# Kernel optimization log

Hardware: AMD Instinct MI355X
Metric: run time of the kernel (lower is better)

## Reference

```python
import jax, jax.numpy as jnp
import numpy as np

# Real spherical harmonics constants (torch-ngp / instant-ngp shencoder convention)
C0 = 0.28209479177387814
C1 = 0.48860251190291987
C2_0 = 1.0925484305920792
C2_2 = 0.94617469575755997
C2_2b = 0.31539156525251999
C2_4 = 0.54627421529603959
C3_0 = 0.59004358992664352
C3_1 = 2.8906114426405538
C3_2 = 0.45704579946446572
C3_3 = 0.3731763325901154
C3_5 = 1.4453057213202769


def sh_encode_deg4(d):
    # d: [..., 3] normalized directions -> [..., 16]
    x, y, z = d[..., 0], d[..., 1], d[..., 2]
    x2, y2, z2 = x * x, y * y, z * z
    xy, yz, xz = x * y, y * z, x * z
    terms = [
        jnp.full_like(x, C0),            # l=0
        -C1 * y,                          # l=1
        C1 * z,
        -C1 * x,
        C2_0 * xy,                        # l=2
        -C2_0 * yz,
        C2_2 * z2 - C2_2b,
        -C2_0 * xz,
        C2_4 * (x2 - y2),
        C3_0 * y * (-3.0 * x2 + y2),      # l=3
        C3_1 * xy * z,
        C3_2 * y * (1.0 - 5.0 * z2),
        C3_3 * z * (5.0 * z2 - 3.0),
        C3_2 * x * (1.0 - 5.0 * z2),
        C3_5 * z * (x2 - y2),
        C3_0 * x * (-x2 + 3.0 * y2),
    ]
    return jnp.stack(terms, axis=-1)


def setup_inputs() -> dict:
    key = jax.random.key(0)
    d = jax.random.normal(key, (4194304, 3), dtype=jnp.float32)
    d = d / jnp.linalg.norm(d, axis=-1, keepdims=True)  # module expects normalized dirs
    return {"direction": d}


def reference(direction):
    # SHEncoder.forward with degree=4: [..., 3] -> [..., 16]
    prefix = direction.shape[:-1]
    out = sh_encode_deg4(direction.reshape(-1, 3))
    return out.reshape(prefix + (16,))
```

## Files before the change

kernel.cpp:

```cpp
#include <hip/hip_runtime.h>
#include <hip/hip_bf16.h>


#define C0    0.28209479177387814f
#define C1    0.48860251190291987f
#define C2_0  1.0925484305920792f
#define C2_2  0.94617469575755997f
#define C2_2b 0.31539156525251999f
#define C2_4  0.54627421529603959f
#define C3_0  0.59004358992664352f
#define C3_1  2.8906114426405538f
#define C3_2  0.45704579946446572f
#define C3_3  0.3731763325901154f
#define C3_5  1.4453057213202769f

#define BLK 256

__global__ __launch_bounds__(BLK) void sh_encode_kernel(
    const float* __restrict__ din, float* __restrict__ dout, int N) {
    __shared__ float4 s4[BLK * 4];

    const int tid  = threadIdx.x;
    const int base = blockIdx.x * BLK;
    const int i    = base + tid;

    float x = 0.f, y = 0.f, z = 0.f;
    if (i < N) {
        const float* p = din + (size_t)3 * i;
        x = p[0]; y = p[1]; z = p[2];
    }

    const float x2 = x * x, y2 = y * y, z2 = z * z;
    const float xy = x * y, yz = y * z, xz = x * z;

    float t[16];
    t[0]  = C0;
    t[1]  = -C1 * y;
    t[2]  =  C1 * z;
    t[3]  = -C1 * x;
    t[4]  =  C2_0 * xy;
    t[5]  = -C2_0 * yz;
    t[6]  =  C2_2 * z2 - C2_2b;
    t[7]  = -C2_0 * xz;
    t[8]  =  C2_4 * (x2 - y2);
    t[9]  =  C3_0 * y * (-3.0f * x2 + y2);
    t[10] =  C3_1 * xy * z;
    t[11] =  C3_2 * y * (1.0f - 5.0f * z2);
    t[12] =  C3_3 * z * (5.0f * z2 - 3.0f);
    t[13] =  C3_2 * x * (1.0f - 5.0f * z2);
    t[14] =  C3_5 * z * (x2 - y2);
    t[15] =  C3_0 * x * (-x2 + 3.0f * y2);

    const int sw = (tid >> 1) & 3;
    #pragma unroll
    for (int g = 0; g < 4; ++g) {
        s4[tid * 4 + (g ^ sw)] =
            make_float4(t[4 * g], t[4 * g + 1], t[4 * g + 2], t[4 * g + 3]);
    }

    __syncthreads();

    float4* outb4 = (float4*)(dout + (size_t)base * 16);
    #pragma unroll
    for (int it = 0; it < 4; ++it) {
        const int e4 = it * BLK + tid;
        const int p  = e4 >> 2;
        const int q  = e4 & 3;
        if (base + p < N)
            outb4[e4] = s4[p * 4 + (q ^ ((p >> 1) & 3))];
    }
}

extern "C" void kernel_launch(void* const* d_in, const int* in_sizes, int n_in,
                              void* d_out, int out_size, void* d_ws, size_t ws_size,
                              hipStream_t stream) {
    const float* din = (const float*)d_in[0];
    float* dout      = (float*)d_out;
    const int N      = in_sizes[0] / 3;
    const int blocks = (N + BLK - 1) / BLK;
    sh_encode_kernel<<<blocks, BLK, 0, stream>>>(din, dout, N);
}
```

Measured before the change: 57.84 us.

## Use per-wave LDS transpose, nontemporal stores, and drop block barrier

Each wave now stages and transposes only its own 64 points in a private slice of shared memory, so the block-wide __syncthreads is replaced by a wave-local LDS wait. Output stores use nontemporal hints so the large streaming write bypasses cache retention, and full blocks skip the per-element bounds checks. The approach relies on wave-level lockstep for LDS visibility, which holds for 64-wide AMD waves but is an implicit assumption.

```diff
diff --git a/kernel.cpp b/kernel.cpp
--- a/kernel.cpp
+++ b/kernel.cpp
@@ -16,16 +16,21 @@
 
 #define BLK 256
 
+typedef float f4 __attribute__((ext_vector_type(4)));
+
 __global__ __launch_bounds__(BLK) void sh_encode_kernel(
     const float* __restrict__ din, float* __restrict__ dout, int N) {
-    __shared__ float4 s4[BLK * 4];
+    __shared__ f4 s4[BLK * 4];
 
     const int tid  = threadIdx.x;
+    const int lane = tid & 63;
+    const int wave = tid >> 6;
     const int base = blockIdx.x * BLK;
     const int i    = base + tid;
+    const bool full = (base + BLK) <= N;
 
     float x = 0.f, y = 0.f, z = 0.f;
-    if (i < N) {
+    if (full || i < N) {
         const float* p = din + (size_t)3 * i;
         x = p[0]; y = p[1]; z = p[2];
     }
@@ -51,23 +56,34 @@
     t[14] =  C3_5 * z * (x2 - y2);
     t[15] =  C3_0 * x * (-x2 + 3.0f * y2);
 
-    const int sw = (tid >> 1) & 3;
+    f4* ws = s4 + (wave << 8);
+    const int sw = (lane >> 1) & 3;
     #pragma unroll
     for (int g = 0; g < 4; ++g) {
-        s4[tid * 4 + (g ^ sw)] =
-            make_float4(t[4 * g], t[4 * g + 1], t[4 * g + 2], t[4 * g + 3]);
+        f4 v = {t[4 * g], t[4 * g + 1], t[4 * g + 2], t[4 * g + 3]};
+        ws[(lane << 2) + (g ^ sw)] = v;
     }
 
-    __syncthreads();
+    asm volatile("s_waitcnt lgkmcnt(0)" ::: "memory");
 
-    float4* outb4 = (float4*)(dout + (size_t)base * 16);
-    #pragma unroll
-    for (int it = 0; it < 4; ++it) {
-        const int e4 = it * BLK + tid;
-        const int p  = e4 >> 2;
-        const int q  = e4 & 3;
-        if (base + p < N)
-            outb4[e4] = s4[p * 4 + (q ^ ((p >> 1) & 3))];
+    const int wbase = base + (wave << 6);
+    f4* outw = (f4*)dout + ((size_t)wbase << 2);
+    if (full) {
+        #pragma unroll
+        for (int it = 0; it < 4; ++it) {
+            const int e4 = (it << 6) + lane;
+            const int p  = e4 >> 2, q = e4 & 3;
+            __builtin_nontemporal_store(ws[(p << 2) + (q ^ ((p >> 1) & 3))],
+                                        &outw[e4]);
+        }
+    } else {
+        for (int it = 0; it < 4; ++it) {
+            const int e4 = (it << 6) + lane;
+            const int p  = e4 >> 2, q = e4 & 3;
+            if (wbase + p < N)
+                __builtin_nontemporal_store(ws[(p << 2) + (q ^ ((p >> 1) & 3))],
+                                            &outw[e4]);
+        }
     }
 }
 
```

New measurement: 50.20 us. 1.15x faster.
